# Optimization experiments

Measured on AMD Instinct MI355X. Metric: run time of the kernel, lower is better.

The kernel has to match this reference:

```python
import jax, jax.numpy as jnp
import numpy as np
from jax import lax

DIM = 192
NUM_HEADS = 4
HEAD_DIM = DIM // NUM_HEADS
EPS_NORM = 1e-12  # F.normalize default eps
EPS_TEMP = 1e-06


def setup_inputs() -> dict:
    key = jax.random.key(0)
    k1, k2, k3, k4 = jax.random.split(key, 4)
    b, c, h, w = 2, DIM, 192, 192
    x = jax.random.normal(k1, (b, c, h, w), dtype=jnp.float32)
    # conv weights, fan-in scaled for sane magnitudes
    w_qkv = jax.random.normal(k2, (3 * DIM, DIM), dtype=jnp.float32) / np.sqrt(DIM)
    w_dw = jax.random.normal(k3, (3 * DIM, 1, 3, 3), dtype=jnp.float32) / 3.0
    w_proj = jax.random.normal(k4, (DIM, DIM), dtype=jnp.float32) / np.sqrt(DIM)
    log_temperature = jnp.zeros((NUM_HEADS, 1, 1), dtype=jnp.float32)
    return {"x": x, "w_qkv": w_qkv, "w_dw": w_dw, "w_proj": w_proj,
            "log_temperature": log_temperature}


def _l2norm_lastdim(t):
    n = jnp.sqrt(jnp.sum(t * t, axis=-1, keepdims=True))
    return t / jnp.maximum(n, EPS_NORM)


def reference(x, w_qkv, w_dw, w_proj, log_temperature):
    b, c, h, w = x.shape
    hw = h * w
    # 1x1 conv (pointwise GEMM over channels)
    qkv = jnp.einsum('oc,bchw->bohw', w_qkv, x)
    # depthwise 3x3 conv, padding=1
    qkv = lax.conv_general_dilated(
        qkv, w_dw, window_strides=(1, 1), padding='SAME',
        feature_group_count=3 * c,
        dimension_numbers=('NCHW', 'OIHW', 'NCHW'))
    q, k, v = jnp.split(qkv, 3, axis=1)
    # [b, heads, head_dim, hw]
    q = q.reshape(b, NUM_HEADS, HEAD_DIM, hw)
    k = k.reshape(b, NUM_HEADS, HEAD_DIM, hw)
    v = v.reshape(b, NUM_HEADS, HEAD_DIM, hw)
    q = _l2norm_lastdim(q)
    k = _l2norm_lastdim(k)
    # channel-wise attention: [b, heads, head_dim, head_dim]
    attn = jnp.einsum('bhdn,bhen->bhde', q, k)
    temperature = jax.nn.softplus(log_temperature) + EPS_TEMP  # [heads,1,1]
    attn = attn * temperature[None]
    attn = jax.nn.softmax(attn, axis=-1)
    out = jnp.einsum('bhde,bhen->bhdn', attn, v)
    out = out.reshape(b, c, h, w)
    return jnp.einsum('oc,bchw->bohw', w_proj, out)
```

## Files before the change

### kernel.cpp

```cpp
#include <hip/hip_runtime.h>
#include <math.h>

#define HW 36864
#define CC 192

typedef __attribute__((ext_vector_type(4))) float f32x4;
typedef __attribute__((ext_vector_type(8))) short bf16x8;

__device__ __forceinline__ float bf2f(unsigned short u) {
    return __uint_as_float(((unsigned int)u) << 16);
}
__device__ __forceinline__ unsigned short f2bf(float f) {
    unsigned int u = __float_as_uint(f);
    unsigned int r = (u + 0x7fffu + ((u >> 16) & 1u)) >> 16;
    return (unsigned short)r;
}

template<bool XF32, bool OUTBF>
__global__ __launch_bounds__(256, 3) void gemm_rpa(
    const unsigned short* __restrict__ A,
    const void* __restrict__ Xv,
    void* __restrict__ Outv,
    long aBatchStride, long xBatchStride, long oBatchStride)
{
    const int n0 = blockIdx.x * 64;
    const int b  = blockIdx.y;
    const int mbase = blockIdx.z * 192;
    const int tid = threadIdx.x;
    const int lane = tid & 63;
    const int wave = tid >> 6;
    const int ml = lane & 15, qk = lane >> 4;

    __shared__ __attribute__((aligned(16))) unsigned short Xs[64 * 202];

    const unsigned short* Ab = A + (long)b * aBatchStride;
    bf16x8 afr[3][6];
#pragma unroll
    for (int f = 0; f < 3; ++f) {
        const unsigned short* row = Ab + (long)(mbase + wave * 48 + f * 16 + ml) * 192 + qk * 8;
#pragma unroll
        for (int kk = 0; kk < 6; ++kk)
            afr[f][kk] = *(const bf16x8*)(row + kk * 32);
    }

    const int kp = tid & 31;
    const int nc = tid >> 5;
    for (int k0 = 0; k0 < 192; k0 += 64) {
        const int k = k0 + 2 * kp;
        unsigned int pk[8];
        if (XF32) {
            const float* xp = (const float*)Xv + (long)b * xBatchStride + (long)k * HW + n0 + nc * 8;
            float4 a0 = *(const float4*)(xp);
            float4 a1 = *(const float4*)(xp + 4);
            float4 b0 = *(const float4*)(xp + HW);
            float4 b1 = *(const float4*)(xp + HW + 4);
            float lo[8] = {a0.x, a0.y, a0.z, a0.w, a1.x, a1.y, a1.z, a1.w};
            float hi[8] = {b0.x, b0.y, b0.z, b0.w, b1.x, b1.y, b1.z, b1.w};
#pragma unroll
            for (int j = 0; j < 8; ++j)
                pk[j] = (unsigned int)f2bf(lo[j]) | ((unsigned int)f2bf(hi[j]) << 16);
        } else {
            const unsigned short* xp = (const unsigned short*)Xv + (long)b * xBatchStride + (long)k * HW + n0 + nc * 8;
            int4 r0 = *(const int4*)(xp);
            int4 r1 = *(const int4*)(xp + HW);
            const unsigned short* u0 = (const unsigned short*)&r0;
            const unsigned short* u1 = (const unsigned short*)&r1;
#pragma unroll
            for (int j = 0; j < 8; ++j)
                pk[j] = (unsigned int)u0[j] | ((unsigned int)u1[j] << 16);
        }
#pragma unroll
        for (int j = 0; j < 8; ++j)
            *(unsigned int*)&Xs[(nc * 8 + j) * 202 + k] = pk[j];
    }
    __syncthreads();

    f32x4 acc[3][4];
#pragma unroll
    for (int f = 0; f < 3; ++f)
#pragma unroll
        for (int s = 0; s < 4; ++s)
            acc[f][s] = (f32x4){0.f, 0.f, 0.f, 0.f};

#pragma unroll
    for (int s = 0; s < 4; ++s) {
#pragma unroll
        for (int kk = 0; kk < 6; ++kk) {
            bf16x8 bfr;
            {
                const unsigned short* p = &Xs[(s * 16 + ml) * 202 + kk * 32 + qk * 8];
                union { bf16x8 v; unsigned int u[4]; } tmp;
                tmp.u[0] = *(const unsigned int*)(p + 0);
                tmp.u[1] = *(const unsigned int*)(p + 2);
                tmp.u[2] = *(const unsigned int*)(p + 4);
                tmp.u[3] = *(const unsigned int*)(p + 6);
                bfr = tmp.v;
            }
#pragma unroll
            for (int f = 0; f < 3; ++f)
                acc[f][s] = __builtin_amdgcn_mfma_f32_16x16x32_bf16(afr[f][kk], bfr, acc[f][s], 0, 0, 0);
        }
    }

#pragma unroll
    for (int f = 0; f < 3; ++f) {
        if (OUTBF) {
            unsigned short* Out = (unsigned short*)Outv + (long)b * oBatchStride;
#pragma unroll
            for (int s = 0; s < 4; ++s) {
                const int gm = mbase + wave * 48 + f * 16 + qk * 4;
                const int gn = n0 + s * 16 + ml;
#pragma unroll
                for (int i = 0; i < 4; ++i)
                    Out[(long)(gm + i) * HW + gn] = f2bf(acc[f][s][i]);
            }
        } else {
            float* Out = (float*)Outv + (long)b * oBatchStride;
#pragma unroll
            for (int s = 0; s < 4; ++s) {
                const int gm = mbase + wave * 48 + f * 16 + qk * 4;
                const int gn = n0 + s * 16 + ml;
#pragma unroll
                for (int i = 0; i < 4; ++i)
                    Out[(long)(gm + i) * HW + gn] = acc[f][s][i];
            }
        }
    }
}

__global__ __launch_bounds__(256) void dwconv_kernel(
    const unsigned short* __restrict__ qkv,
    const float* __restrict__ wdw,
    unsigned short* __restrict__ dwout,
    float* __restrict__ ssq)
{
    const int ht = blockIdx.x;
    const int ch = blockIdx.y;
    const int b  = blockIdx.z;
    const int tid = threadIdx.x;
    const int lane = tid & 63;
    const int h0 = ht * 8;
    const int t  = tid & 31;
    const int hh = tid >> 5;
    const bool active = (t < 24);

    const float* wp = wdw + ch * 9;
    const float w00 = wp[0], w01 = wp[1], w02 = wp[2];
    const float w10 = wp[3], w11 = wp[4], w12 = wp[5];
    const float w20 = wp[6], w21 = wp[7], w22 = wp[8];

    const long chbase = (long)(b * 576 + ch) * HW;

    float x[3][8];
#pragma unroll
    for (int dy = 0; dy < 3; ++dy) {
        const int hr = h0 + hh + dy - 1;
        int4 ld = make_int4(0, 0, 0, 0);
        if (active && hr >= 0 && hr < 192)
            ld = *(const int4*)(qkv + chbase + (long)hr * 192 + t * 8);
        const unsigned short* u = (const unsigned short*)&ld;
#pragma unroll
        for (int j = 0; j < 8; ++j) x[dy][j] = bf2f(u[j]);
    }

    float lft[3], rgt[3];
#pragma unroll
    for (int dy = 0; dy < 3; ++dy) {
        float l = __shfl(x[dy][7], lane - 1, 64);
        float r = __shfl(x[dy][0], lane + 1, 64);
        lft[dy] = (t == 0) ? 0.f : l;
        rgt[dy] = (t >= 23) ? 0.f : r;
    }

    float acc[8];
#pragma unroll
    for (int j = 0; j < 8; ++j) {
        float a0 = (j == 0) ? lft[0] : x[0][j - 1];
        float a2 = (j == 7) ? rgt[0] : x[0][j + 1];
        float b0 = (j == 0) ? lft[1] : x[1][j - 1];
        float b2 = (j == 7) ? rgt[1] : x[1][j + 1];
        float c0 = (j == 0) ? lft[2] : x[2][j - 1];
        float c2 = (j == 7) ? rgt[2] : x[2][j + 1];
        acc[j] = w00 * a0 + w01 * x[0][j] + w02 * a2
               + w10 * b0 + w11 * x[1][j] + w12 * b2
               + w20 * c0 + w21 * x[2][j] + w22 * c2;
    }

    if (active) {
        int4 st;
        unsigned short* u = (unsigned short*)&st;
#pragma unroll
        for (int j = 0; j < 8; ++j) u[j] = f2bf(acc[j]);
        *(int4*)(dwout + chbase + (long)(h0 + hh) * 192 + t * 8) = st;
    }

    if (ch < 384) {
        float mysq = 0.f;
        if (active) {
#pragma unroll
            for (int j = 0; j < 8; ++j) mysq += acc[j] * acc[j];
        }
#pragma unroll
        for (int off = 32; off > 0; off >>= 1) mysq += __shfl_xor(mysq, off, 64);
        __shared__ float red[4];
        if (lane == 0) red[tid >> 6] = mysq;
        __syncthreads();
        if (tid == 0) atomicAdd(&ssq[b * 384 + ch], red[0] + red[1] + red[2] + red[3]);
    }
}

__global__ __launch_bounds__(64) void gram_kernel(
    const unsigned short* __restrict__ dwb, float* __restrict__ gram)
{
    const int chunk = blockIdx.x;
    const int bh = blockIdx.y;
    const int b = bh >> 2, h = bh & 3;
    const int lane = threadIdx.x;
    const int row = lane & 15, qk = lane >> 4;
    const long n0 = (long)chunk * 512;

    const unsigned short* qb = dwb + (long)(b * 576 + h * 48) * HW + n0;
    const unsigned short* kb = dwb + (long)(b * 576 + 192 + h * 48) * HW + n0;

    f32x4 acc[3][3];
#pragma unroll
    for (int f = 0; f < 3; ++f)
#pragma unroll
        for (int g = 0; g < 3; ++g) acc[f][g] = (f32x4){0.f, 0.f, 0.f, 0.f};

    for (int kk = 0; kk < 512; kk += 32) {
        const int col = kk + qk * 8;
        bf16x8 aq[3], bk[3];
#pragma unroll
        for (int f = 0; f < 3; ++f) aq[f] = *(const bf16x8*)(qb + (long)(f * 16 + row) * HW + col);
#pragma unroll
        for (int g = 0; g < 3; ++g) bk[g] = *(const bf16x8*)(kb + (long)(g * 16 + row) * HW + col);
#pragma unroll
        for (int f = 0; f < 3; ++f)
#pragma unroll
            for (int g = 0; g < 3; ++g)
                acc[f][g] = __builtin_amdgcn_mfma_f32_16x16x32_bf16(aq[f], bk[g], acc[f][g], 0, 0, 0);
    }

    float* gb = gram + bh * 2304;
#pragma unroll
    for (int f = 0; f < 3; ++f)
#pragma unroll
        for (int g = 0; g < 3; ++g)
#pragma unroll
            for (int i = 0; i < 4; ++i)
                atomicAdd(&gb[(f * 16 + qk * 4 + i) * 48 + g * 16 + row], acc[f][g][i]);
}

__global__ __launch_bounds__(64) void attn_kernel(
    const float* __restrict__ gram, const float* __restrict__ ssq,
    const float* __restrict__ lt, float* __restrict__ attn)
{
    const int bh = blockIdx.x;
    const int b = bh >> 2, h = bh & 3;
    const int d = threadIdx.x;
    if (d >= 48) return;
    const float temp = log1pf(expf(lt[h])) + 1e-6f;
    const float invq = 1.f / fmaxf(sqrtf(ssq[b * 384 + h * 48 + d]), 1e-12f);
    float p[48];
    float mx = -1e30f;
#pragma unroll
    for (int e = 0; e < 48; ++e) {
        float invk = 1.f / fmaxf(sqrtf(ssq[b * 384 + 192 + h * 48 + e]), 1e-12f);
        float g = gram[bh * 2304 + d * 48 + e] * invq * invk * temp;
        p[e] = g;
        mx = fmaxf(mx, g);
    }
    float sum = 0.f;
#pragma unroll
    for (int e = 0; e < 48; ++e) { float x = expf(p[e] - mx); p[e] = x; sum += x; }
    const float inv = 1.f / sum;
#pragma unroll
    for (int e = 0; e < 48; ++e) attn[bh * 2304 + d * 48 + e] = p[e] * inv;
}

__global__ __launch_bounds__(192) void mproj_kernel(
    const float* __restrict__ wproj, const float* __restrict__ attn,
    unsigned short* __restrict__ Mb)
{
    const int o = blockIdx.x;
    const int b = blockIdx.y;
    const int he = threadIdx.x;
    const int h = he / 48, e = he - h * 48;
    const float* ar = attn + ((b * 4 + h) * 48) * 48 + e;
    const float* wr = wproj + o * 192 + h * 48;
    float acc = 0.f;
#pragma unroll
    for (int d = 0; d < 48; ++d) acc += wr[d] * ar[d * 48];
    Mb[(long)(b * 192 + o) * 192 + he] = f2bf(acc);
}

__global__ void cvt_bf16_kernel(const float* __restrict__ in,
                                unsigned short* __restrict__ out, int n)
{
    int i = blockIdx.x * 256 + threadIdx.x;
    if (i < n) out[i] = f2bf(in[i]);
}

extern "C" void kernel_launch(void* const* d_in, const int* in_sizes, int n_in,
                              void* d_out, int out_size, void* d_ws, size_t ws_size,
                              hipStream_t stream)
{
    const float* x      = (const float*)d_in[0];
    const float* w_qkv  = (const float*)d_in[1];
    const float* w_dw   = (const float*)d_in[2];
    const float* w_proj = (const float*)d_in[3];
    const float* lt     = (const float*)d_in[4];

    char* ws = (char*)d_ws;
    unsigned short* wqkv_b = (unsigned short*)(ws + 0);
    float* gram            = (float*)(ws + 221184);
    float* ssq             = (float*)(ws + 294912);
    float* attn            = (float*)(ws + 297984);
    unsigned short* Mb     = (unsigned short*)(ws + 371712);
    unsigned short* qkvb   = (unsigned short*)(ws + 524288);
    unsigned short* dwb    = (unsigned short*)(ws + 524288 + 84934656ll);

    hipMemsetAsync(gram, 0, 73728 + 3072, stream);

    cvt_bf16_kernel<<<dim3((110592 + 255) / 256), 256, 0, stream>>>(w_qkv, wqkv_b, 110592);

    gemm_rpa<true, true><<<dim3(576, 2, 3), 256, 0, stream>>>(
        wqkv_b, (const void*)x, (void*)qkvb,
        0L, (long)192 * HW, (long)576 * HW);

    dwconv_kernel<<<dim3(24, 576, 2), 256, 0, stream>>>(qkvb, w_dw, dwb, ssq);

    gram_kernel<<<dim3(72, 8), 64, 0, stream>>>(dwb, gram);

    attn_kernel<<<dim3(8), 64, 0, stream>>>(gram, ssq, lt, attn);

    mproj_kernel<<<dim3(192, 2), 192, 0, stream>>>(w_proj, attn, Mb);

    gemm_rpa<false, false><<<dim3(576, 2, 1), 256, 0, stream>>>(
        Mb, (const void*)(dwb + (long)384 * HW), d_out,
        (long)192 * 192, (long)576 * HW, (long)192 * HW);
}
```

Baseline: 269.1 us.

## Pre-transpose GEMM inputs to pixel-major bf16 and drop LDS staging in GEMMs

Adds a transpose kernel that converts x (and later the v slice) into a pixel-major bf16 layout, so the pointwise GEMMs can load MFMA B-fragments straight from global memory without LDS staging or syncs. The GEMM tile shrinks to 48 columns with higher occupancy, and the gram kernel is split into four times as many smaller chunks for more parallelism. The cost is two extra full-tensor transpose passes through HBM, plus the gram atomics rising fourfold.

```diff
diff --git a/kernel.cpp b/kernel.cpp
--- a/kernel.cpp
+++ b/kernel.cpp
@@ -16,86 +16,95 @@
     return (unsigned short)r;
 }
 
-template<bool XF32, bool OUTBF>
-__global__ __launch_bounds__(256, 3) void gemm_rpa(
+template<bool INF32>
+__global__ __launch_bounds__(256) void xpose_kernel(
+    const void* __restrict__ src, unsigned short* __restrict__ dst,
+    long srcBatchStride)
+{
+    const int n0  = blockIdx.x * 64;
+    const int ch0 = blockIdx.y * 64;
+    const int b   = blockIdx.z;
+    const int tid = threadIdx.x;
+    const int chp = tid >> 3;
+    const int nq  = tid & 7;
+
+    __shared__ unsigned int T[64 * 33];
+
+    const long rbase = (long)b * srcBatchStride + (long)(ch0 + 2 * chp) * HW + n0 + nq * 8;
+    unsigned int pk[8];
+    if (INF32) {
+        const float* s0 = (const float*)src + rbase;
+        float4 a0 = *(const float4*)(s0);
+        float4 a1 = *(const float4*)(s0 + 4);
+        float4 b0 = *(const float4*)(s0 + HW);
+        float4 b1 = *(const float4*)(s0 + HW + 4);
+        float lo[8] = {a0.x, a0.y, a0.z, a0.w, a1.x, a1.y, a1.z, a1.w};
+        float hi[8] = {b0.x, b0.y, b0.z, b0.w, b1.x, b1.y, b1.z, b1.w};
+#pragma unroll
+        for (int j = 0; j < 8; ++j)
+            pk[j] = (unsigned int)f2bf(lo[j]) | ((unsigned int)f2bf(hi[j]) << 16);
+    } else {
+        const unsigned short* s0 = (const unsigned short*)src + rbase;
+        int4 r0 = *(const int4*)(s0);
+        int4 r1 = *(const int4*)(s0 + HW);
+        const unsigned short* u0 = (const unsigned short*)&r0;
+        const unsigned short* u1 = (const unsigned short*)&r1;
+#pragma unroll
+        for (int j = 0; j < 8; ++j)
+            pk[j] = (unsigned int)u0[j] | ((unsigned int)u1[j] << 16);
+    }
+#pragma unroll
+    for (int j = 0; j < 8; ++j)
+        T[(nq * 8 + j) * 33 + chp] = pk[j];
+    __syncthreads();
+
+#pragma unroll
+    for (int it = 0; it < 2; ++it) {
+        const int slot = it * 256 + tid;
+        const int n = slot >> 3, seg = slot & 7;
+        uint4 v = *(const uint4*)&T[n * 33 + seg * 4];
+        *(uint4*)(dst + ((long)b * HW + n0 + n) * 192 + ch0 + seg * 8) = v;
+    }
+}
+
+template<bool OUTBF>
+__global__ __launch_bounds__(256, 4) void gemm_nols(
     const unsigned short* __restrict__ A,
-    const void* __restrict__ Xv,
+    const unsigned short* __restrict__ XT,
     void* __restrict__ Outv,
-    long aBatchStride, long xBatchStride, long oBatchStride)
-{
-    const int n0 = blockIdx.x * 64;
+    long aBatchStride, long oBatchStride)
+{
+    const int n0 = blockIdx.x * 48;
     const int b  = blockIdx.y;
-    const int mbase = blockIdx.z * 192;
-    const int tid = threadIdx.x;
-    const int lane = tid & 63;
-    const int wave = tid >> 6;
+    const int mbase = blockIdx.z * 192 + (int)(threadIdx.x >> 6) * 48;
+    const int lane = threadIdx.x & 63;
     const int ml = lane & 15, qk = lane >> 4;
-
-    __shared__ __attribute__((aligned(16))) unsigned short Xs[64 * 202];
 
     const unsigned short* Ab = A + (long)b * aBatchStride;
     bf16x8 afr[3][6];
 #pragma unroll
     for (int f = 0; f < 3; ++f) {
-        const unsigned short* row = Ab + (long)(mbase + wave * 48 + f * 16 + ml) * 192 + qk * 8;
+        const unsigned short* row = Ab + (long)(mbase + f * 16 + ml) * 192 + qk * 8;
 #pragma unroll
         for (int kk = 0; kk < 6; ++kk)
             afr[f][kk] = *(const bf16x8*)(row + kk * 32);
     }
 
-    const int kp = tid & 31;
-    const int nc = tid >> 5;
-    for (int k0 = 0; k0 < 192; k0 += 64) {
-        const int k = k0 + 2 * kp;
-        unsigned int pk[8];
-        if (XF32) {
-            const float* xp = (const float*)Xv + (long)b * xBatchStride + (long)k * HW + n0 + nc * 8;
-            float4 a0 = *(const float4*)(xp);
-            float4 a1 = *(const float4*)(xp + 4);
-            float4 b0 = *(const float4*)(xp + HW);
-            float4 b1 = *(const float4*)(xp + HW + 4);
-            float lo[8] = {a0.x, a0.y, a0.z, a0.w, a1.x, a1.y, a1.z, a1.w};
-            float hi[8] = {b0.x, b0.y, b0.z, b0.w, b1.x, b1.y, b1.z, b1.w};
-#pragma unroll
-            for (int j = 0; j < 8; ++j)
-                pk[j] = (unsigned int)f2bf(lo[j]) | ((unsigned int)f2bf(hi[j]) << 16);
-        } else {
-            const unsigned short* xp = (const unsigned short*)Xv + (long)b * xBatchStride + (long)k * HW + n0 + nc * 8;
-            int4 r0 = *(const int4*)(xp);
-            int4 r1 = *(const int4*)(xp + HW);
-            const unsigned short* u0 = (const unsigned short*)&r0;
-            const unsigned short* u1 = (const unsigned short*)&r1;
-#pragma unroll
-            for (int j = 0; j < 8; ++j)
-                pk[j] = (unsigned int)u0[j] | ((unsigned int)u1[j] << 16);
-        }
-#pragma unroll
-        for (int j = 0; j < 8; ++j)
-            *(unsigned int*)&Xs[(nc * 8 + j) * 202 + k] = pk[j];
-    }
-    __syncthreads();
-
-    f32x4 acc[3][4];
+    const unsigned short* Xb = XT + ((long)b * HW + n0) * 192;
+
+    f32x4 acc[3][3];
 #pragma unroll
     for (int f = 0; f < 3; ++f)
 #pragma unroll
-        for (int s = 0; s < 4; ++s)
+        for (int s = 0; s < 3; ++s)
             acc[f][s] = (f32x4){0.f, 0.f, 0.f, 0.f};
 
 #pragma unroll
-    for (int s = 0; s < 4; ++s) {
+    for (int s = 0; s < 3; ++s) {
+        const unsigned short* xrow = Xb + (long)(s * 16 + ml) * 192 + qk * 8;
 #pragma unroll
         for (int kk = 0; kk < 6; ++kk) {
-            bf16x8 bfr;
-            {
-                const unsigned short* p = &Xs[(s * 16 + ml) * 202 + kk * 32 + qk * 8];
-                union { bf16x8 v; unsigned int u[4]; } tmp;
-                tmp.u[0] = *(const unsigned int*)(p + 0);
-                tmp.u[1] = *(const unsigned int*)(p + 2);
-                tmp.u[2] = *(const unsigned int*)(p + 4);
-                tmp.u[3] = *(const unsigned int*)(p + 6);
-                bfr = tmp.v;
-            }
+            bf16x8 bfr = *(const bf16x8*)(xrow + kk * 32);
 #pragma unroll
             for (int f = 0; f < 3; ++f)
                 acc[f][s] = __builtin_amdgcn_mfma_f32_16x16x32_bf16(afr[f][kk], bfr, acc[f][s], 0, 0, 0);
@@ -107,8 +116,8 @@
         if (OUTBF) {
             unsigned short* Out = (unsigned short*)Outv + (long)b * oBatchStride;
 #pragma unroll
-            for (int s = 0; s < 4; ++s) {
-                const int gm = mbase + wave * 48 + f * 16 + qk * 4;
+            for (int s = 0; s < 3; ++s) {
+                const int gm = mbase + f * 16 + qk * 4;
                 const int gn = n0 + s * 16 + ml;
 #pragma unroll
                 for (int i = 0; i < 4; ++i)
@@ -117,8 +126,8 @@
         } else {
             float* Out = (float*)Outv + (long)b * oBatchStride;
 #pragma unroll
-            for (int s = 0; s < 4; ++s) {
-                const int gm = mbase + wave * 48 + f * 16 + qk * 4;
+            for (int s = 0; s < 3; ++s) {
+                const int gm = mbase + f * 16 + qk * 4;
                 const int gn = n0 + s * 16 + ml;
 #pragma unroll
                 for (int i = 0; i < 4; ++i)
@@ -217,7 +226,7 @@
     const int b = bh >> 2, h = bh & 3;
     const int lane = threadIdx.x;
     const int row = lane & 15, qk = lane >> 4;
-    const long n0 = (long)chunk * 512;
+    const long n0 = (long)chunk * 128;
 
     const unsigned short* qb = dwb + (long)(b * 576 + h * 48) * HW + n0;
     const unsigned short* kb = dwb + (long)(b * 576 + 192 + h * 48) * HW + n0;
@@ -228,7 +237,8 @@
 #pragma unroll
         for (int g = 0; g < 3; ++g) acc[f][g] = (f32x4){0.f, 0.f, 0.f, 0.f};
 
-    for (int kk = 0; kk < 512; kk += 32) {
+#pragma unroll
+    for (int kk = 0; kk < 128; kk += 32) {
         const int col = kk + qk * 8;
         bf16x8 aq[3], bk[3];
 #pragma unroll
@@ -320,24 +330,30 @@
     unsigned short* Mb     = (unsigned short*)(ws + 371712);
     unsigned short* qkvb   = (unsigned short*)(ws + 524288);
     unsigned short* dwb    = (unsigned short*)(ws + 524288 + 84934656ll);
+    unsigned short* xT = dwb;
+    unsigned short* vT = qkvb;
 
     hipMemsetAsync(gram, 0, 73728 + 3072, stream);
 
     cvt_bf16_kernel<<<dim3((110592 + 255) / 256), 256, 0, stream>>>(w_qkv, wqkv_b, 110592);
 
-    gemm_rpa<true, true><<<dim3(576, 2, 3), 256, 0, stream>>>(
-        wqkv_b, (const void*)x, (void*)qkvb,
-        0L, (long)192 * HW, (long)576 * HW);
+    xpose_kernel<true><<<dim3(576, 3, 2), 256, 0, stream>>>(
+        (const void*)x, xT, (long)192 * HW);
+
+    gemm_nols<true><<<dim3(768, 2, 3), 256, 0, stream>>>(
+        wqkv_b, xT, (void*)qkvb, 0L, (long)576 * HW);
 
     dwconv_kernel<<<dim3(24, 576, 2), 256, 0, stream>>>(qkvb, w_dw, dwb, ssq);
 
-    gram_kernel<<<dim3(72, 8), 64, 0, stream>>>(dwb, gram);
+    gram_kernel<<<dim3(288, 8), 64, 0, stream>>>(dwb, gram);
+
+    xpose_kernel<false><<<dim3(576, 3, 2), 256, 0, stream>>>(
+        (const void*)(dwb + (long)384 * HW), vT, (long)576 * HW);
 
     attn_kernel<<<dim3(8), 64, 0, stream>>>(gram, ssq, lt, attn);
 
     mproj_kernel<<<dim3(192, 2), 192, 0, stream>>>(w_proj, attn, Mb);
 
-    gemm_rpa<false, false><<<dim3(576, 2, 1), 256, 0, stream>>>(
-        Mb, (const void*)(dwb + (long)384 * HW), d_out,
-        (long)192 * 192, (long)576 * HW, (long)192 * HW);
-}
+    gemm_nols<false><<<dim3(768, 2, 1), 256, 0, stream>>>(
+        Mb, vT, d_out, (long)192 * 192, (long)192 * HW);
+}
```

After: 346.6 us. +28.8%, slower.
